# Kernel tuning notes

Measured on AMD Instinct MI355X. Metric: run time of the kernel, lower is better.

Reference implementation:

```python
import jax, jax.numpy as jnp
import numpy as np

B, G = 32, 100                      # batch, max ground-truth boxes per image
LEVELS = [(80, 8), (40, 16), (20, 32)]  # (grid_size, stride) for 640x640 input -> 8400 anchors
NUM_CLASSES = 1


def _grids():
    xs, ys, ss = [], [], []
    for n, s in LEVELS:
        yy, xx = np.meshgrid(np.arange(n), np.arange(n), indexing="ij")
        xs.append(xx.reshape(-1)); ys.append(yy.reshape(-1)); ss.append(np.full(n * n, s))
    f = lambda a: jnp.asarray(np.concatenate(a), jnp.float32)[None]
    return f(xs), f(ys), f(ss)


def setup_inputs() -> dict:
    key = jax.random.key(0)
    k1, k2, k3, k4, k5, k6 = jax.random.split(key, 6)
    x_shifts, y_shifts, strides = _grids()
    A = x_shifts.shape[1]
    # decoded predictions: cx,cy in image, positive w,h; obj/cls are raw logits
    cxy = jax.random.uniform(k1, (B, A, 2), minval=0.0, maxval=640.0)
    wh = jax.random.uniform(k2, (B, A, 2), minval=4.0, maxval=128.0)
    objcls = jax.random.normal(k3, (B, A, 1 + NUM_CLASSES))
    outputs = jnp.concatenate([cxy, wh, objcls], -1)
    # labels: (class, cx, cy, w, h), zero-padded past the per-image gt count
    gxy = jax.random.uniform(k4, (B, G, 2), minval=32.0, maxval=608.0)
    gwh = jax.random.uniform(k5, (B, G, 2), minval=8.0, maxval=128.0)
    ngt = jax.random.randint(k6, (B,), 1, G + 1)
    valid = (jnp.arange(G)[None, :] < ngt[:, None]).astype(jnp.float32)[..., None]
    labels = jnp.concatenate([jnp.zeros((B, G, 1)), gxy, gwh], -1) * valid
    return {"outputs": outputs, "labels": labels, "x_shifts": x_shifts,
            "y_shifts": y_shifts, "expanded_strides": strides}


def _pairwise_iou_cxcywh(a, b):  # a [G,4] gt, b [A,4] preds -> [G,A]
    tl = jnp.maximum(a[:, None, :2] - a[:, None, 2:] / 2, b[None, :, :2] - b[None, :, 2:] / 2)
    br = jnp.minimum(a[:, None, :2] + a[:, None, 2:] / 2, b[None, :, :2] + b[None, :, 2:] / 2)
    inter = jnp.prod(jnp.maximum(br - tl, 0.0), -1)
    area_a = jnp.prod(a[:, 2:], -1)[:, None]
    area_b = jnp.prod(b[:, 2:], -1)[None, :]
    return inter / (area_a + area_b - inter + 1e-12)


def _assign_one(out, lab, xc, yc, st):
    """SimOTA assignment for one image. out [A,6], lab [G,5], xc/yc/st [A]."""
    bbox, obj, cls = out[:, :4], out[:, 4:5], out[:, 5:]
    valid_gt = lab.sum(-1) > 0                       # [G] mirrors nlabel logic
    gt = lab[:, 1:5]
    gt_cls = lab[:, 0].astype(jnp.int32)
    gcx, gcy, gw, gh = gt[:, 0:1], gt[:, 1:2], gt[:, 2:3], gt[:, 3:4]
    # anchor center inside gt box
    in_box = ((xc[None] > gcx - gw / 2) & (xc[None] < gcx + gw / 2) &
              (yc[None] > gcy - gh / 2) & (yc[None] < gcy + gh / 2))
    # anchor center within 2.5*stride of gt center
    r = 2.5 * st[None]
    in_ctr = (jnp.abs(xc[None] - gcx) < r) & (jnp.abs(yc[None] - gcy) < r)
    in_box &= valid_gt[:, None]
    in_ctr &= valid_gt[:, None]
    fg = (in_box | in_ctr).any(0)                    # [A] candidate fg anchors
    geo = in_box & in_ctr                            # [G,A]
    pair_ok = fg[None, :] & valid_gt[:, None]
    ious = _pairwise_iou_cxcywh(gt, bbox)            # [G,A]
    iou_m = jnp.where(pair_ok, ious, 0.0)
    # cls cost: BCE( sqrt(sigmoid(cls)*sigmoid(obj)), one_hot(gt_cls) )
    p = jnp.sqrt(jax.nn.sigmoid(cls) * jax.nn.sigmoid(obj))      # [A,C]
    t = jax.nn.one_hot(gt_cls, NUM_CLASSES)                       # [G,C]
    cls_cost = -(t[:, None, :] * jnp.log(p[None] + 1e-9) +
                 (1.0 - t[:, None, :]) * jnp.log(1.0 - p[None] + 1e-9)).sum(-1)
    cost = cls_cost + 3.0 * (-jnp.log(ious + 1e-8)) + 1e5 * (~geo)
    cost = jnp.where(pair_ok, cost, 1e9)             # exclude non-fg / padded gts
    # dynamic-k: k_g = clamp(sum(top-10 ious), min 1)
    topk_ious = jax.lax.top_k(iou_m, 10)[0]
    dyn_k = jnp.maximum(topk_ious.sum(-1).astype(jnp.int32), 1)  # [G]
    # rank anchors per gt by ascending cost; pick rank < dyn_k
    ranks = jnp.argsort(jnp.argsort(cost, axis=1), axis=1)
    matching = (ranks < dyn_k[:, None]) & pair_ok
    # resolve anchors matched to >1 gt: keep the min-cost gt
    cnt = matching.sum(0)
    best_gt = jnp.argmin(cost, 0)                    # [A]
    matching = jnp.where((cnt > 1)[None, :], jnp.arange(G)[:, None] == best_gt[None, :], matching)
    fg_final = matching.any(0)                       # [A]
    pred_iou = (matching.astype(ious.dtype) * ious).sum(0)       # [A]
    matched_gt = jnp.argmax(matching, 0)             # [A]
    cls_t = jax.nn.one_hot(gt_cls[matched_gt], NUM_CLASSES) * pred_iou[:, None]
    cls_t = jnp.where(fg_final[:, None], cls_t, 0.0)
    return fg_final, cls_t


def reference(outputs, labels, x_shifts, y_shifts, expanded_strides):
    st = expanded_strides[0]
    xc = (x_shifts[0] + 0.5) * st
    yc = (y_shifts[0] + 0.5) * st
    fg, cls_t = jax.vmap(lambda o, l: _assign_one(o, l, xc, yc, st))(outputs, labels)
    # assignment runs under no_grad in the original
    fg = jax.lax.stop_gradient(fg)
    cls_t = jax.lax.stop_gradient(cls_t)
    logits = outputs[:, :, 5:]                       # [B,A,C]
    bce = cls_t * jax.nn.softplus(-logits) + (1.0 - cls_t) * jax.nn.softplus(logits)
    num_fg = jnp.maximum(fg.sum().astype(jnp.float32), 1.0)
    return (bce * fg[..., None]).sum() / num_fg
```

## Files before the change

kernel.cpp:

```cpp
#include <hip/hip_runtime.h>
#include <hip/hip_bf16.h>
#include <stdint.h>

#define BB 32
#define GG 100
#define AA 8400
#define TPB 256
#define NCH 33
#define TKB 512
#define BA (BB*AA)
#define NG (BB*GG)
#define NB2 (BB*GG)
#define NITB 17
#define PCAP 8416
#define GCAP 128
#define SCAP (GG*10)

typedef __hip_bfloat16 bf16;

struct P {
  const void *outs, *labs, *ss;
  float4 *box4, *gtb, *gtc;
  float2 *aux2;
  float *pcc, *zl;
  int   *sel_a;
  float *sel_iou;
  int   *cnt, *own;
  float *pb, *pf;
  int *gmax;
  float *out;
};

__device__ __forceinline__ int dtypeFlag(const void* ss){
  return (((const uint32_t*)ss)[0] == 0x41000000u) ? 1 : 0;
}
__device__ __forceinline__ float ld(const void* p, int i, int isf32){
  return isf32 ? ((const float*)p)[i] : __bfloat162float(((const bf16*)p)[i]);
}
__device__ __forceinline__ void ageom(int a, float& xc, float& yc, float& r){
  int x, y, s;
  if (a < 6400){ x = a % 80; y = a / 80; s = 8; }
  else if (a < 8000){ int q = a - 6400; x = q % 40; y = q / 40; s = 16; }
  else { int q = a - 8000; x = q % 20; y = q / 20; s = 32; }
  float fs = (float)s;
  xc = ((float)x + 0.5f) * fs;
  yc = ((float)y + 0.5f) * fs;
  r  = 2.5f * fs;
}
__device__ __forceinline__ uint32_t apack2(int a){
  int x, y, s, lvl;
  if (a < 6400){ x = a % 80; y = a / 80; s = 8; lvl = 0; }
  else if (a < 8000){ int q = a - 6400; x = q % 40; y = q / 40; s = 16; lvl = 1; }
  else { int q = a - 8000; x = q % 20; y = q / 20; s = 32; lvl = 2; }
  return (uint32_t)(x*s + s/2) | ((uint32_t)(y*s + s/2) << 10) | ((uint32_t)lvl << 20);
}

__global__ __launch_bounds__(TPB) void kA(P p){
  __shared__ float4 s_gtb[GG], s_gtc[GG];
  __shared__ float s_o[TPB*6];
  __shared__ int s_ng;
  int t = threadIdx.x;
  int c = blockIdx.x, b = blockIdx.y;
  int isf = dtypeFlag(p.ss);
  if (t == 0) s_ng = 0;
  {
    int s = c*TPB + t;
    if (s < SCAP) p.sel_a[b*SCAP + s] = -1;
  }
  int nel = min(TPB*6, AA*6 - c*(TPB*6));
  if (isf){
    const float4* src = (const float4*)((const float*)p.outs + (size_t)b*AA*6 + (size_t)c*(TPB*6));
    float4* dst = (float4*)s_o;
    for (int i = t; i < nel/4; i += TPB) dst[i] = src[i];
  } else {
    const uint4* src = (const uint4*)((const bf16*)p.outs + (size_t)b*AA*6 + (size_t)c*(TPB*6));
    for (int i = t; i < nel/8; i += TPB){
      uint4 u = src[i];
      int o = i*8;
      s_o[o+0]=__uint_as_float(u.x<<16); s_o[o+1]=__uint_as_float(u.x&0xffff0000u);
      s_o[o+2]=__uint_as_float(u.y<<16); s_o[o+3]=__uint_as_float(u.y&0xffff0000u);
      s_o[o+4]=__uint_as_float(u.z<<16); s_o[o+5]=__uint_as_float(u.z&0xffff0000u);
      s_o[o+6]=__uint_as_float(u.w<<16); s_o[o+7]=__uint_as_float(u.w&0xffff0000u);
    }
  }
  __syncthreads();
  if (t < GG){
    int i = b*GG + t;
    float l0 = ld(p.labs, i*5  , isf);
    float gcx= ld(p.labs, i*5+1, isf);
    float gcy= ld(p.labs, i*5+2, isf);
    float gw = ld(p.labs, i*5+3, isf);
    float gh = ld(p.labs, i*5+4, isf);
    int valid = (l0+gcx+gcy+gw+gh) > 0.f;
    float4 vb = make_float4(gcx-gw*0.5f, gcy-gh*0.5f, gcx+gw*0.5f, gcy+gh*0.5f);
    float4 vc = make_float4(gcx, gcy, gw*gh, valid ? 1.f : 0.f);
    s_gtb[t] = vb; s_gtc[t] = vc;
    if (c == 0){ p.gtb[i] = vb; p.gtc[i] = vc; }
    if (valid) atomicMax(&s_ng, t+1);
  }
  __syncthreads();
  int ng = s_ng;
  if (c == 0 && t == 0) p.gmax[b] = ng;
  int a = c*TPB + t;
  if (a < AA){
    float cx=s_o[t*6], cy=s_o[t*6+1], w=s_o[t*6+2], h=s_o[t*6+3], ob=s_o[t*6+4], cl=s_o[t*6+5];
    int idx = b*AA + a;
    p.box4[idx] = make_float4(cx-w*0.5f, cy-h*0.5f, cx+w*0.5f, cy+h*0.5f);
    float so = 1.f/(1.f+expf(-ob));
    float sc = 1.f/(1.f+expf(-cl));
    float pccv = -logf(sqrtf(sc*so) + 1e-9f);
    float xc, yc, r; ageom(a, xc, yc, r);
    int fg = 0;
    for (int g = 0; g < ng; ++g){
      float4 gb = s_gtb[g], gc = s_gtc[g];
      bool inb = (xc>gb.x)&&(xc<gb.z)&&(yc>gb.y)&&(yc<gb.w);
      bool inc = (fabsf(xc-gc.x)<r)&&(fabsf(yc-gc.y)<r);
      fg |= (gc.w != 0.f) && (inb||inc);
    }
    float area = w*h;
    p.aux2[idx] = make_float2(fg ? area : -area, __uint_as_float(apack2(a)));
    p.pcc[idx] = pccv;
    p.zl [idx] = cl;
    p.cnt[idx] = 0;
    p.own[idx] = 0x7fffffff;
  }
}

__global__ __launch_bounds__(TKB) void kB(P p){
  __shared__ float s_pos[PCAP];
  __shared__ float s_gcost[GCAP];
  __shared__ int   s_gpos[GCAP];
  __shared__ int   s_pcnt, s_gcnt;
  int t = threadIdx.x;
  int lane = t & 63, wid = t >> 6;
  int item = blockIdx.x;
  int b = item / GG, g = item - b*GG;
  if (t == 0){ s_pcnt = 0; s_gcnt = 0; }
  float4 gc = p.gtc[b*GG+g];
  if (gc.w == 0.f) return;
  float4 gb = p.gtb[b*GG+g];
  float glx=gb.x, gly=gb.y, ghx=gb.z, ghy=gb.w, gcx=gc.x, gcy=gc.y, ga=gc.z;
  int base = b*AA;
  unsigned long long lmlt = (1ull<<lane) - 1ull;
  __syncthreads();

  for (int it = 0; it < NITB; ++it){
    int pos = it*TKB + t;
    bool ovl = false, geo = false;
    float v = 0.f, cst = 0.f;
    if (pos < AA){
      float2 aux = p.aux2[base+pos];
      float4 bx  = p.box4[base+pos];
      bool fg = aux.x > 0.f;
      uint32_t u = __float_as_uint(aux.y);
      float xc = (float)(u & 1023u), yc = (float)((u>>10)&1023u);
      float r  = (float)(20u << (u>>20));
      bool inb = (xc>glx)&&(xc<ghx)&&(yc>gly)&&(yc<ghy);
      geo = inb && (fabsf(xc-gcx)<r) && (fabsf(yc-gcy)<r);
      float tlx=fmaxf(glx,bx.x), tly=fmaxf(gly,bx.y);
      float brx=fminf(ghx,bx.z), bry=fminf(ghy,bx.w);
      float iw=brx-tlx, ih=bry-tly;
      ovl = fg && (iw>0.f) && (ih>0.f);
      if (ovl | geo){
        float area = fabsf(aux.x);
        float inter = fmaxf(iw,0.f)*fmaxf(ih,0.f);
        v = inter/(ga + area - inter + 1e-12f);
        if (geo) cst = p.pcc[base+pos] + 3.f*(-logf(v+1e-8f));
      }
    }
    unsigned long long m1 = __ballot(ovl);
    if (m1){
      int ldr = (int)(__ffsll(m1)-1);
      int off;
      if (lane == ldr) off = atomicAdd(&s_pcnt, __popcll(m1));
      off = __shfl(off, ldr);
      if (ovl) s_pos[off + __popcll(m1 & lmlt)] = v;
    }
    unsigned long long m2 = __ballot(geo);
    if (m2){
      int ldr = (int)(__ffsll(m2)-1);
      int off;
      if (lane == ldr) off = atomicAdd(&s_gcnt, __popcll(m2));
      off = __shfl(off, ldr);
      if (geo){
        int q = off + __popcll(m2 & lmlt);
        s_gcost[q] = cst; s_gpos[q] = pos;
      }
    }
  }
  __syncthreads();
  if (wid) return;

  int pcnt = s_pcnt, gcnt = s_gcnt;

  float lmax = -1.f;
  for (int i = lane; i < pcnt; i += 64) lmax = fmaxf(lmax, s_pos[i]);
  float sum = 0.f;
  for (int k = 0; k < 10; ++k){
    float gv = lmax;
#pragma unroll
    for (int off=32; off; off>>=1) gv = fmaxf(gv, __shfl_xor(gv, off));
    if (gv <= 0.f) break;
    sum += gv;
    unsigned long long ms = __ballot(lmax == gv);
    if ((int)(__ffsll(ms)-1) == lane){
      bool fnd = false; float nl = -1.f;
      for (int i = lane; i < pcnt; i += 64){
        float vv = s_pos[i];
        if (!fnd && vv == gv){ fnd = true; vv = -1.f; s_pos[i] = vv; }
        nl = fmaxf(nl, vv);
      }
      lmax = nl;
    }
  }
  int dk = (int)sum; if (dk<1) dk=1; if (dk>10) dk=10;

  float c0=3.0e38f, c1=3.0e38f; int p0=0x7fffffff, p1=0x7fffffff;
  if (lane < gcnt){ c0 = s_gcost[lane]; p0 = s_gpos[lane]; }
  if (lane+64 < gcnt){ c1 = s_gcost[lane+64]; p1 = s_gpos[lane+64]; }
  if (c1 < c0 || (c1==c0 && p1<p0)){
    float tc=c0; c0=c1; c1=tc; int tp=p0; p0=p1; p1=tp;
  }
  int mysel = -1, take = 0;
  for (int k = 0; k < dk; ++k){
    float gv=c0; int gi=p0;
#pragma unroll
    for (int off=32; off; off>>=1){
      float ov=__shfl_xor(gv,off); int oi=__shfl_xor(gi,off);
      if (ov<gv || (ov==gv && oi<gi)){ gv=ov; gi=oi; }
    }
    if (gv >= 2.9e38f) break;
    if (lane == k) mysel = gi;
    take++;
    if (c0==gv && p0==gi){ c0=c1; p0=p1; c1=3.0e38f; p1=0x7fffffff; }
  }

  float lastc = -3.0e38f; int lastp = -1;
  for (int k = take; k < dk; ++k){
    float bc = 3.0e38f; int bp = 0x7fffffff;
    int n64 = (AA + 63) >> 6;
    for (int it = 0; it < n64; ++it){
      int pos = (it<<6) + lane;
      if (pos < AA){
        float2 aux = p.aux2[base+pos];
        bool fg = aux.x > 0.f;
        if (fg){
          uint32_t u = __float_as_uint(aux.y);
          float xc = (float)(u & 1023u), yc = (float)((u>>10)&1023u);
          float r  = (float)(20u << (u>>20));
          bool inb = (xc>glx)&&(xc<ghx)&&(yc>gly)&&(yc<ghy);
          bool geo2 = inb && (fabsf(xc-gcx)<r) && (fabsf(yc-gcy)<r);
          if (!geo2){
            float4 bx = p.box4[base+pos];
            float tlx=fmaxf(glx,bx.x), tly=fmaxf(gly,bx.y);
            float brx=fminf(ghx,bx.z), bry=fminf(ghy,bx.w);
            float iw=fmaxf(brx-tlx,0.f), ih=fmaxf(bry-tly,0.f);
            float inter=iw*ih;
            float area = fabsf(aux.x);
            float v = inter/(ga + area - inter + 1e-12f);
            float cst = p.pcc[base+pos] + 3.f*(-logf(v+1e-8f)) + 100000.f;
            bool gt = (cst > lastc) || (cst == lastc && pos > lastp);
            bool lt = (cst < bc)   || (cst == bc   && pos < bp);
            if (gt && lt){ bc = cst; bp = pos; }
          }
        }
      }
    }
#pragma unroll
    for (int off=32; off; off>>=1){
      float ov=__shfl_xor(bc,off); int oi=__shfl_xor(bp,off);
      if (ov<bc || (ov==bc && oi<bp)){ bc=ov; bp=oi; }
    }
    if (bc >= 2.9e38f) break;
    if (lane == k) mysel = bp;
    lastc = bc; lastp = bp;
  }

  if (mysel >= 0){
    int a = mysel;
    float4 bx = p.box4[base+a];
    float area = fabsf(p.aux2[base+a].x);
    float tlx=fmaxf(glx,bx.x), tly=fmaxf(gly,bx.y);
    float brx=fminf(ghx,bx.z), bry=fminf(ghy,bx.w);
    float iw=fmaxf(brx-tlx,0.f), ih=fmaxf(bry-tly,0.f);
    float inter=iw*ih;
    float iou=inter/(ga + area - inter + 1e-12f);
    int slot = g*10 + lane;
    p.sel_a [b*SCAP + slot] = a;
    p.sel_iou[b*SCAP + slot] = iou;
    atomicAdd(&p.cnt[base+a], 1);
    atomicMin(&p.own[base+a], slot);
  }
}

__global__ __launch_bounds__(64) void kR(P p){
  int lane = threadIdx.x;
  int item = blockIdx.x;
  int b = item / GG, g = item - b*GG;
  int base = b*AA;
  int a = -1, cgt = 0;
  bool ownr = false;
  float iouv = 0.f;
  if (lane < 10){
    int slot = g*10 + lane;
    a = p.sel_a[b*SCAP + slot];
    if (a >= 0 && p.own[base+a] == slot){
      ownr = true;
      cgt = p.cnt[base+a];
      iouv = p.sel_iou[b*SCAP + slot];
    }
  }
  unsigned long long cm = __ballot(ownr && cgt > 1);
  if (cm){
    int ng = p.gmax[b];
    while (cm){
      int s = (int)(__ffsll(cm)-1); cm &= cm - 1ull;
      int aa = __shfl(a, s);
      float area = fabsf(p.aux2[base+aa].x);
      float pccv = p.pcc[base+aa];
      float4 bx = p.box4[base+aa];
      float xc,yc,r; ageom(aa,xc,yc,r);
      float bc = 3.9e38f, bi = 0.f; int bg = 0x7fffffff;
      for (int g2 = lane; g2 < ng; g2 += 64){
        float4 gbb = p.gtb[b*GG+g2], gcc = p.gtc[b*GG+g2];
        float cost, iou2 = 0.f;
        if (gcc.w != 0.f){
          float tlx=fmaxf(gbb.x,bx.x), tly=fmaxf(gbb.y,bx.y);
          float brx=fminf(gbb.z,bx.z), bry=fminf(gbb.w,bx.w);
          float iw=fmaxf(brx-tlx,0.f), ih=fmaxf(bry-tly,0.f);
          float inter=iw*ih;
          iou2 = inter/(gcc.z + area - inter + 1e-12f);
          bool inb=(xc>gbb.x)&&(xc<gbb.z)&&(yc>gbb.y)&&(yc<gbb.w);
          bool inc=(fabsf(xc-gcc.x)<r)&&(fabsf(yc-gcc.y)<r);
          cost = pccv + 3.f*(-logf(iou2+1e-8f)) + ((inb&&inc)?0.f:100000.f);
        } else cost = 1e9f;
        if (cost < bc){ bc=cost; bi=iou2; bg=g2; }
      }
#pragma unroll
      for (int off=32; off; off>>=1){
        float oc=__shfl_xor(bc,off), oi=__shfl_xor(bi,off);
        int og=__shfl_xor(bg,off);
        if (oc<bc || (oc==bc && og<bg)){ bc=oc; bi=oi; bg=og; }
      }
      if (lane == s) iouv = bi;
    }
  }
  float bce = 0.f, fgv = 0.f;
  if (lane < 10 && ownr){
    float z = p.zl[base+a];
    float e = expf(-fabsf(z));
    float spz = fmaxf(z,0.f)+log1pf(e);
    float spn = fmaxf(-z,0.f)+log1pf(e);
    bce = iouv*spn + (1.f-iouv)*spz;
    fgv = 1.f;
  }
#pragma unroll
  for (int off=32; off; off>>=1){
    bce += __shfl_xor(bce, off);
    fgv += __shfl_xor(fgv, off);
  }
  if (lane == 0){ p.pb[item] = bce; p.pf[item] = fgv; }
}

__global__ __launch_bounds__(TPB) void kD(P p){
  int t = threadIdx.x;
  float sb=0.f, sf=0.f;
  for (int i = t; i < NB2; i += TPB){ sb += p.pb[i]; sf += p.pf[i]; }
#pragma unroll
  for (int off=32; off; off>>=1){
    sb += __shfl_xor(sb, off);
    sf += __shfl_xor(sf, off);
  }
  __shared__ float s_b[4], s_f[4];
  int lane = t & 63, wid = t >> 6;
  if (lane==0){ s_b[wid]=sb; s_f[wid]=sf; }
  __syncthreads();
  if (t==0){
    float tb=s_b[0]+s_b[1]+s_b[2]+s_b[3];
    float tf=s_f[0]+s_f[1]+s_f[2]+s_f[3];
    p.out[0] = tb / fmaxf(tf, 1.f);
  }
}

extern "C" void kernel_launch(void* const* d_in, const int* in_sizes, int n_in,
                              void* d_out, int out_size, void* d_ws, size_t ws_size,
                              hipStream_t stream) {
  P p;
  p.outs = d_in[0];
  p.labs = d_in[1];
  p.ss   = d_in[4];
  char* w = (char*)d_ws;
  p.box4  = (float4*)w; w += (size_t)BA*sizeof(float4);
  p.gtb   = (float4*)w; w += (size_t)NG*sizeof(float4);
  p.gtc   = (float4*)w; w += (size_t)NG*sizeof(float4);
  p.aux2  = (float2*)w; w += (size_t)BA*sizeof(float2);
  p.pcc   = (float*)w;  w += (size_t)BA*sizeof(float);
  p.zl    = (float*)w;  w += (size_t)BA*sizeof(float);
  p.sel_a = (int*)w;    w += (size_t)BB*SCAP*sizeof(int);
  p.sel_iou=(float*)w;  w += (size_t)BB*SCAP*sizeof(float);
  p.cnt   = (int*)w;    w += (size_t)BA*sizeof(int);
  p.own   = (int*)w;    w += (size_t)BA*sizeof(int);
  p.gmax  = (int*)w;    w += (size_t)BB*sizeof(int);
  p.pb    = (float*)w;  w += (size_t)NB2*sizeof(float);
  p.pf    = (float*)w;  w += (size_t)NB2*sizeof(float);
  p.out   = (float*)d_out;

  kA<<<dim3(NCH, BB), TPB, 0, stream>>>(p);
  kB<<<BB*GG, TKB, 0, stream>>>(p);
  kR<<<NB2, 64, 0, stream>>>(p);
  kD<<<1, TPB, 0, stream>>>(p);
}
```

Before: 151.3 us.

## Bin predicted boxes into spatial grid cells and scan only nearby cells per GT

Predicted boxes are bucketed into a 10x10 grid of 64-pixel cells by their center, and a new kernel scatters them into cell-sorted arrays. The per-GT kernel then scans only the cell rows that can overlap the GT box instead of all 8400 anchors. Geometric center candidates are enumerated directly from the anchor grid bounds per level instead of tested exhaustively. This cuts the per-GT scan work but adds a binning/scatter kernel, extra workspace traffic, and relies on box half-size bounds (w,h up to 128) for correctness of the cell margin.

Measured after the change: 148.6 us. About the same (-1.8%).

```diff
diff --git a/kernel.cpp b/kernel.cpp
--- a/kernel.cpp
+++ b/kernel.cpp
@@ -11,7 +11,8 @@
 #define BA (BB*AA)
 #define NG (BB*GG)
 #define NB2 (BB*GG)
-#define NITB 17
+#define NCX 10
+#define NCELL 100
 #define PCAP 8416
 #define GCAP 128
 #define SCAP (GG*10)
@@ -23,6 +24,11 @@
   float4 *box4, *gtb, *gtc;
   float2 *aux2;
   float *pcc, *zl;
+  int   *cellid;
+  int   *chunkcell;
+  int   *bstart, *btot;
+  float *barea;
+  float4 *bb4;
   int   *sel_a;
   float *sel_iou;
   int   *cnt, *own;
@@ -59,10 +65,12 @@
   __shared__ float4 s_gtb[GG], s_gtc[GG];
   __shared__ float s_o[TPB*6];
   __shared__ int s_ng;
+  __shared__ int s_h[NCELL];
   int t = threadIdx.x;
   int c = blockIdx.x, b = blockIdx.y;
   int isf = dtypeFlag(p.ss);
   if (t == 0) s_ng = 0;
+  if (t < NCELL) s_h[t] = 0;
   {
     int s = c*TPB + t;
     if (s < SCAP) p.sel_a[b*SCAP + s] = -1;
@@ -123,75 +131,158 @@
     p.zl [idx] = cl;
     p.cnt[idx] = 0;
     p.own[idx] = 0x7fffffff;
-  }
-}
-
-__global__ __launch_bounds__(TKB) void kB(P p){
+    int cxi = min(NCX-1, (int)(cx * 0.015625f));
+    int cyi = min(NCX-1, (int)(cy * 0.015625f));
+    int cell = cyi*NCX + cxi;
+    p.cellid[idx] = cell;
+    atomicAdd(&s_h[cell], 1);
+  }
+  __syncthreads();
+  if (t < NCELL) p.chunkcell[(b*NCH + c)*NCELL + t] = s_h[t];
+}
+
+__global__ __launch_bounds__(TPB) void kY(P p){
+  __shared__ int s_cnt[NCELL], s_pre[NCELL], s_cur[NCELL], s_sta[NCELL];
+  int t = threadIdx.x, c = blockIdx.x, b = blockIdx.y;
+  if (t < NCELL){
+    int tot = 0, pre = 0;
+    for (int k = 0; k < NCH; ++k){
+      int v = p.chunkcell[(b*NCH + k)*NCELL + t];
+      tot += v;
+      if (k < c) pre += v;
+    }
+    s_cnt[t] = tot; s_pre[t] = pre;
+  }
+  __syncthreads();
+  if (t == 0){
+    int run = 0;
+    for (int j = 0; j < NCELL; ++j){
+      s_sta[j] = run;
+      s_cur[j] = run + s_pre[j];
+      run += s_cnt[j];
+    }
+  }
+  __syncthreads();
+  if (c == 0 && t < NCELL){
+    p.bstart[b*NCELL + t] = s_sta[t];
+    p.btot  [b*NCELL + t] = s_cnt[t];
+  }
+  int a = c*TPB + t;
+  if (a < AA){
+    int idx = b*AA + a;
+    int cell = p.cellid[idx];
+    int q = atomicAdd(&s_cur[cell], 1);
+    p.barea[b*AA + q] = p.aux2[idx].x;
+    p.bb4  [b*AA + q] = p.box4[idx];
+  }
+}
+
+__global__ __launch_bounds__(TKB) void kB2(P p){
   __shared__ float s_pos[PCAP];
   __shared__ float s_gcost[GCAP];
   __shared__ int   s_gpos[GCAP];
-  __shared__ int   s_pcnt, s_gcnt;
+  __shared__ int   s_pcnt;
   int t = threadIdx.x;
   int lane = t & 63, wid = t >> 6;
   int item = blockIdx.x;
   int b = item / GG, g = item - b*GG;
-  if (t == 0){ s_pcnt = 0; s_gcnt = 0; }
-  float4 gc = p.gtc[b*GG+g];
+  if (t == 0) s_pcnt = 0;
+  float4 gc = p.gtc[item];
   if (gc.w == 0.f) return;
-  float4 gb = p.gtb[b*GG+g];
+  float4 gb = p.gtb[item];
   float glx=gb.x, gly=gb.y, ghx=gb.z, ghy=gb.w, gcx=gc.x, gcy=gc.y, ga=gc.z;
   int base = b*AA;
   unsigned long long lmlt = (1ull<<lane) - 1ull;
   __syncthreads();
 
-  for (int it = 0; it < NITB; ++it){
-    int pos = it*TKB + t;
-    bool ovl = false, geo = false;
-    float v = 0.f, cst = 0.f;
-    if (pos < AA){
-      float2 aux = p.aux2[base+pos];
-      float4 bx  = p.box4[base+pos];
-      bool fg = aux.x > 0.f;
-      uint32_t u = __float_as_uint(aux.y);
-      float xc = (float)(u & 1023u), yc = (float)((u>>10)&1023u);
-      float r  = (float)(20u << (u>>20));
-      bool inb = (xc>glx)&&(xc<ghx)&&(yc>gly)&&(yc<ghy);
-      geo = inb && (fabsf(xc-gcx)<r) && (fabsf(yc-gcy)<r);
-      float tlx=fmaxf(glx,bx.x), tly=fmaxf(gly,bx.y);
-      float brx=fminf(ghx,bx.z), bry=fminf(ghy,bx.w);
-      float iw=brx-tlx, ih=bry-tly;
-      ovl = fg && (iw>0.f) && (ih>0.f);
-      if (ovl | geo){
-        float area = fabsf(aux.x);
-        float inter = fmaxf(iw,0.f)*fmaxf(ih,0.f);
-        v = inter/(ga + area - inter + 1e-12f);
-        if (geo) cst = p.pcc[base+pos] + 3.f*(-logf(v+1e-8f));
-      }
-    }
-    unsigned long long m1 = __ballot(ovl);
-    if (m1){
-      int ldr = (int)(__ffsll(m1)-1);
-      int off;
-      if (lane == ldr) off = atomicAdd(&s_pcnt, __popcll(m1));
-      off = __shfl(off, ldr);
-      if (ovl) s_pos[off + __popcll(m1 & lmlt)] = v;
-    }
-    unsigned long long m2 = __ballot(geo);
-    if (m2){
-      int ldr = (int)(__ffsll(m2)-1);
-      int off;
-      if (lane == ldr) off = atomicAdd(&s_gcnt, __popcll(m2));
-      off = __shfl(off, ldr);
-      if (geo){
-        int q = off + __popcll(m2 & lmlt);
-        s_gcost[q] = cst; s_gpos[q] = pos;
+  int c0x = max(0, (int)((glx - 64.f) * 0.015625f));
+  int c1x = min(NCX-1, (int)((ghx + 64.f) * 0.015625f));
+  int c0y = max(0, (int)((gly - 64.f) * 0.015625f));
+  int c1y = min(NCX-1, (int)((ghy + 64.f) * 0.015625f));
+
+  for (int cy = c0y; cy <= c1y; ++cy){
+    int cl0 = cy*NCX + c0x, cl1 = cy*NCX + c1x;
+    int s0 = p.bstart[b*NCELL + cl0];
+    int s1 = p.bstart[b*NCELL + cl1] + p.btot[b*NCELL + cl1];
+    int nit = (s1 - s0 + TKB - 1) / TKB;
+    for (int it = 0; it < nit; ++it){
+      int i = s0 + it*TKB + t;
+      bool ovl = false; float v = 0.f;
+      if (i < s1){
+        float ar = p.barea[base + i];
+        if (ar > 0.f){
+          float4 bx = p.bb4[base + i];
+          float tlx=fmaxf(glx,bx.x), tly=fmaxf(gly,bx.y);
+          float brx=fminf(ghx,bx.z), bry=fminf(ghy,bx.w);
+          float iw=brx-tlx, ih=bry-tly;
+          ovl = (iw>0.f) && (ih>0.f);
+          if (ovl){
+            float inter = fmaxf(iw,0.f)*fmaxf(ih,0.f);
+            v = inter/(ga + ar - inter + 1e-12f);
+          }
+        }
+      }
+      unsigned long long m1 = __ballot(ovl);
+      if (m1){
+        int ldr = (int)(__ffsll(m1)-1);
+        int off;
+        if (lane == ldr) off = atomicAdd(&s_pcnt, __popcll(m1));
+        off = __shfl(off, ldr);
+        if (ovl) s_pos[off + __popcll(m1 & lmlt)] = v;
       }
     }
   }
   __syncthreads();
   if (wid) return;
 
-  int pcnt = s_pcnt, gcnt = s_gcnt;
+  int gcnt = 0, lbase = 0;
+  for (int lvl = 0; lvl < 3; ++lvl){
+    int s = 8 << lvl, n = 80 >> lvl;
+    float fr = (float)(20 << lvl);
+    float hs = 0.5f * (float)s;
+    float lox = fmaxf(glx, gcx - fr), hix = fminf(ghx, gcx + fr);
+    float loy = fmaxf(gly, gcy - fr), hiy = fminf(ghy, gcy + fr);
+    int x0 = max(0, (int)((lox - hs) / (float)s));
+    int x1 = min(n-1, (int)((hix - hs) / (float)s) + 1);
+    int y0 = max(0, (int)((loy - hs) / (float)s));
+    int y1 = min(n-1, (int)((hiy - hs) / (float)s) + 1);
+    int W = x1 - x0 + 1, H = y1 - y0 + 1;
+    if (W > 0 && H > 0){
+      int N = W * H;
+      int nit2 = (N + 63) >> 6;
+      for (int it2 = 0; it2 < nit2; ++it2){
+        int i2 = it2*64 + lane;
+        bool geo = false; float cst = 0.f; int aid = 0;
+        if (i2 < N){
+          int xx = x0 + i2 % W, yy = y0 + i2 / W;
+          float xc = (float)(xx*s + (s>>1));
+          float yc = (float)(yy*s + (s>>1));
+          bool inb = (xc>glx)&&(xc<ghx)&&(yc>gly)&&(yc<ghy);
+          geo = inb && (fabsf(xc-gcx)<fr) && (fabsf(yc-gcy)<fr);
+          if (geo){
+            aid = lbase + yy*n + xx;
+            float area = fabsf(p.aux2[base+aid].x);
+            float4 bx = p.box4[base+aid];
+            float tlx=fmaxf(glx,bx.x), tly=fmaxf(gly,bx.y);
+            float brx=fminf(ghx,bx.z), bry=fminf(ghy,bx.w);
+            float iw=brx-tlx, ih=bry-tly;
+            float inter = fmaxf(iw,0.f)*fmaxf(ih,0.f);
+            float v = inter/(ga + area - inter + 1e-12f);
+            cst = p.pcc[base+aid] + 3.f*(-logf(v+1e-8f));
+          }
+        }
+        unsigned long long m2 = __ballot(geo);
+        if (geo){
+          int q = gcnt + __popcll(m2 & lmlt);
+          s_gcost[q] = cst; s_gpos[q] = aid;
+        }
+        gcnt += __popcll(m2);
+      }
+    }
+    lbase += n*n;
+  }
+
+  int pcnt = s_pcnt;
 
   float lmax = -1.f;
   for (int i = lane; i < pcnt; i += 64) lmax = fmaxf(lmax, s_pos[i]);
@@ -393,9 +484,15 @@
   p.box4  = (float4*)w; w += (size_t)BA*sizeof(float4);
   p.gtb   = (float4*)w; w += (size_t)NG*sizeof(float4);
   p.gtc   = (float4*)w; w += (size_t)NG*sizeof(float4);
+  p.bb4   = (float4*)w; w += (size_t)BA*sizeof(float4);
   p.aux2  = (float2*)w; w += (size_t)BA*sizeof(float2);
   p.pcc   = (float*)w;  w += (size_t)BA*sizeof(float);
   p.zl    = (float*)w;  w += (size_t)BA*sizeof(float);
+  p.barea = (float*)w;  w += (size_t)BA*sizeof(float);
+  p.cellid= (int*)w;    w += (size_t)BA*sizeof(int);
+  p.chunkcell=(int*)w;  w += (size_t)BB*NCH*NCELL*sizeof(int);
+  p.bstart= (int*)w;    w += (size_t)BB*NCELL*sizeof(int);
+  p.btot  = (int*)w;    w += (size_t)BB*NCELL*sizeof(int);
   p.sel_a = (int*)w;    w += (size_t)BB*SCAP*sizeof(int);
   p.sel_iou=(float*)w;  w += (size_t)BB*SCAP*sizeof(float);
   p.cnt   = (int*)w;    w += (size_t)BA*sizeof(int);
@@ -406,7 +503,8 @@
   p.out   = (float*)d_out;
 
   kA<<<dim3(NCH, BB), TPB, 0, stream>>>(p);
-  kB<<<BB*GG, TKB, 0, stream>>>(p);
+  kY<<<dim3(NCH, BB), TPB, 0, stream>>>(p);
+  kB2<<<NB2, TKB, 0, stream>>>(p);
   kR<<<NB2, 64, 0, stream>>>(p);
   kD<<<1, TPB, 0, stream>>>(p);
 }
```
